# Kernel optimization log

Measured on AMD Instinct MI355X. Metric: run time of the kernel, lower is better.

Reference implementation:

```python
import jax, jax.numpy as jnp
import numpy as np

DIM = 192
NUM_HEADS = 8
EPS = 1e-12  # F.normalize default eps


def setup_inputs() -> dict:
    key = jax.random.key(0)
    ks = jax.random.split(key, 6)
    b, c, h, w = 8, DIM, 128, 128
    scale = 1.0 / np.sqrt(DIM)  # conv2d default init scale (approx)
    return {
        "input": jax.random.normal(ks[0], (b, c, h, w), dtype=jnp.float32),
        "color": jax.random.normal(ks[1], (b, c, h, w), dtype=jnp.float32),
        "Wq": jax.random.normal(ks[2], (DIM, DIM), dtype=jnp.float32) * scale,
        "Wk": jax.random.normal(ks[3], (DIM, DIM), dtype=jnp.float32) * scale,
        "Wv": jax.random.normal(ks[4], (DIM, DIM), dtype=jnp.float32) * scale,
        "Wo": jax.random.normal(ks[5], (DIM, DIM), dtype=jnp.float32) * scale,
    }


def _proj(x, W):
    # 1x1 conv (bias=False) == channel GEMM: [b,c,h,w] x [out,c] -> [b,out,h,w]
    return jnp.einsum('bchw,oc->bohw', x, W)


def _l2norm(x):
    n = jnp.sqrt(jnp.sum(x * x, axis=-1, keepdims=True))
    return x / jnp.maximum(n, EPS)


def reference(input, color, Wq, Wk, Wv, Wo):
    b, c, h, w = input.shape
    head = NUM_HEADS
    dh = c // head
    hw = h * w
    # q from color, k/v from input
    q = _proj(color, Wq).reshape(b, head, dh, hw)
    k = _proj(input, Wk).reshape(b, head, dh, hw)
    v = _proj(input, Wv).reshape(b, head, dh, hw)
    q = _l2norm(q)
    k = _l2norm(k)
    # transposed (channel) attention: [b,head,dh,dh]
    attn = jnp.einsum('bhcn,bhdn->bhcd', q, k)
    attn = jax.nn.softmax(attn, axis=-1)
    out = jnp.einsum('bhcd,bhdn->bhcn', attn, v)  # [b,head,dh,hw]
    out = out.reshape(b, c, h, w)
    return _proj(out, Wo)
```

## Files before the change

kernel.cpp:

```cpp
#include <hip/hip_runtime.h>
#include <hip/hip_bf16.h>


typedef __attribute__((ext_vector_type(4))) float f32x4;
typedef __attribute__((ext_vector_type(8))) short short8;

#define MFMA16(a, b, c) __builtin_amdgcn_mfma_f32_16x16x32_bf16((a), (b), (c), 0, 0, 0)

__device__ __forceinline__ unsigned int pack_rne(float a, float b) {
  unsigned int ua = __float_as_uint(a), ub = __float_as_uint(b);
  ua += 0x7fffu + ((ua >> 16) & 1u);
  ub += 0x7fffu + ((ub >> 16) & 1u);
  return (ua >> 16) | (ub & 0xffff0000u);
}
__device__ __forceinline__ unsigned short bf16u_rne(float x) {
  unsigned int u = __float_as_uint(x);
  u += 0x7fffu + ((u >> 16) & 1u);
  return (unsigned short)(u >> 16);
}
union S8U { short8 s; unsigned int u[4]; };
__device__ __forceinline__ short8 load_cvt8(const float* p) {
  f32x4 x = *(const f32x4*)p;
  f32x4 y = *(const f32x4*)(p + 4);
  S8U r;
  r.u[0] = pack_rne(x[0], x[1]);
  r.u[1] = pack_rne(x[2], x[3]);
  r.u[2] = pack_rne(y[0], y[1]);
  r.u[3] = pack_rne(y[2], y[3]);
  return r.s;
}

#define HW 16384
#define CDIM 192
#define NB 8
#define GSZ (CDIM * CDIM)
#define NTILE 300
#define FSLOT 24576
#define FSKEW 64
#define BROW 80

__global__ void k0_wvt(const float* __restrict__ Wv, unsigned short* __restrict__ WvT) {
  int idx = blockIdx.x * 256 + threadIdx.x;
  if (idx < CDIM * CDIM) {
    int j = idx / CDIM, cp = idx % CDIM;
    WvT[idx] = bf16u_rne(Wv[(size_t)cp * CDIM + j]);
  }
}

__device__ __forceinline__ short8 bfrag(const char* buf, int row, int lg) {
  return *(const short8*)(buf + row * BROW + lg * 16);
}

__device__ __forceinline__ void stageC(const float* __restrict__ ib,
                                       const float* __restrict__ cb, int col0,
                                       char* fdst, int wave, int lane) {
#pragma unroll
  for (int i = 0; i < 2; ++i) {
    const int g = wave * 2 + i;
    const int tensor = g >= 12;
    const int row = (g - (tensor ? 12 : 0)) * 16 + (lane >> 2);
    const float* T = tensor ? cb : ib;
    const float* gp = T + (size_t)row * HW + col0 + (lane & 3) * 4;
    __builtin_amdgcn_global_load_lds(
        (const __attribute__((address_space(1))) void*)gp,
        (__attribute__((address_space(3))) void*)(fdst + g * 1024), 16, 0, 0);
  }
}

template <int W>
__device__ __forceinline__ void pair_step(const char* bb, f32x4 (&acc)[25],
                                          int l15, int lg) {
  const short8 aT = bfrag(bb, W * 16 + l15, lg);
  const short8 aB = bfrag(bb, (23 - W) * 16 + l15, lg);
#pragma unroll
  for (int ct = W; ct < 24; ++ct) {
    const short8 b = bfrag(bb, ct * 16 + l15, lg);
    acc[ct - W] = MFMA16(aT, b, acc[ct - W]);
    if (ct >= 23 - W) acc[ct + 1] = MFMA16(aB, b, acc[ct + 1]);
  }
}

__device__ __forceinline__ void pair_dispatch(int wp, const char* bb,
                                              f32x4 (&acc)[25], int l15, int lg) {
  switch (wp) {
    case 0: pair_step<0>(bb, acc, l15, lg); break;
    case 1: pair_step<1>(bb, acc, l15, lg); break;
    case 2: pair_step<2>(bb, acc, l15, lg); break;
    case 3: pair_step<3>(bb, acc, l15, lg); break;
    case 4: pair_step<4>(bb, acc, l15, lg); break;
    case 5: pair_step<5>(bb, acc, l15, lg); break;
    case 6: pair_step<6>(bb, acc, l15, lg); break;
    case 7: pair_step<7>(bb, acc, l15, lg); break;
    case 8: pair_step<8>(bb, acc, l15, lg); break;
    case 9: pair_step<9>(bb, acc, l15, lg); break;
    case 10: pair_step<10>(bb, acc, l15, lg); break;
    default: pair_step<11>(bb, acc, l15, lg); break;
  }
}

__global__ __launch_bounds__(768) void gram2_k(const float* __restrict__ input,
                                               const float* __restrict__ color,
                                               unsigned long long* __restrict__ part,
                                               int npart, int ncp) {
  __shared__ __align__(16) char fbuf[2][FSLOT + FSKEW];
  __shared__ __align__(16) char bbuf[384 * BROW];
  const int tid = threadIdx.x, wave = tid >> 6, lane = tid & 63;
  const int l15 = lane & 15, lg = (lane >> 4) & 3;
  const int strip = blockIdx.x, b = blockIdx.y;
  const float* ib = input + (size_t)b * CDIM * HW;
  const float* cb = color + (size_t)b * CDIM * HW;
  const int ch0 = strip * ncp * 2;

  f32x4 acc[25];
#pragma unroll
  for (int i = 0; i < 25; ++i) acc[i] = (f32x4){0.f, 0.f, 0.f, 0.f};

  stageC(ib, cb, (ch0 + 0) * 16, fbuf[0], wave, lane);
  stageC(ib, cb, (ch0 + 1) * 16, fbuf[1], wave, lane);

#pragma unroll 1
  for (int cp = 0; cp < ncp; ++cp) {
    __syncthreads();
    {
      const char* sA = fbuf[0];
      const char* sB = fbuf[1];
#pragma unroll
      for (int u0 = 0; u0 < 2; ++u0) {
        const int u = tid + u0 * 768;
        const int zr = u >> 2, sub = u & 3;
        const char* src = (sub < 2 ? sA : sB) + zr * 64 + (sub & 1) * 32;
        f32x4 x = *(const f32x4*)src;
        f32x4 y = *(const f32x4*)(src + 16);
        S8U pk;
        pk.u[0] = pack_rne(x[0], x[1]);
        pk.u[1] = pack_rne(x[2], x[3]);
        pk.u[2] = pack_rne(y[0], y[1]);
        pk.u[3] = pack_rne(y[2], y[3]);
        *(short8*)(bbuf + zr * BROW + sub * 16) = pk.s;
      }
    }
    __syncthreads();
    if (cp + 1 < ncp) {
      stageC(ib, cb, (ch0 + 2 * cp + 2) * 16, fbuf[0], wave, lane);
      stageC(ib, cb, (ch0 + 2 * cp + 3) * 16, fbuf[1], wave, lane);
    }
    pair_dispatch(wave, bbuf, acc, l15, lg);
  }

  unsigned long long* pbase = part + (size_t)(b * npart + strip) * NTILE * 64;
#pragma unroll
  for (int s = 0; s < 25; ++s) {
    const unsigned long long pk =
        (unsigned long long)pack_rne(acc[s][0], acc[s][1]) |
        ((unsigned long long)pack_rne(acc[s][2], acc[s][3]) << 32);
    pbase[(size_t)(wave * 25 + s) * 64 + lane] = pk;
  }
}

template <int NP>
__global__ __launch_bounds__(256) void reduce_k(const unsigned long long* __restrict__ part,
                                                float* __restrict__ G) {
  const int b = blockIdx.y;
  const int T = blockIdx.x * 4 + (threadIdx.x >> 6);
  const int lane = threadIdx.x & 63;
  const unsigned long long* p = part + ((size_t)b * NP * NTILE + T) * 64 + lane;
  unsigned long long v[NP];
#pragma unroll
  for (int s = 0; s < NP; ++s) v[s] = p[(size_t)s * NTILE * 64];
  float s0 = 0.f, s1 = 0.f, s2 = 0.f, s3 = 0.f;
#pragma unroll
  for (int s = 0; s < NP; ++s) {
    const unsigned int lo = (unsigned int)v[s], hi = (unsigned int)(v[s] >> 32);
    s0 += __uint_as_float(lo << 16);
    s1 += __uint_as_float(lo & 0xffff0000u);
    s2 += __uint_as_float(hi << 16);
    s3 += __uint_as_float(hi & 0xffff0000u);
  }
  const int w = T / 25, s = T % 25;
  int rt, ct;
  if (s <= 23 - w) { rt = w; ct = w + s; }
  else { rt = 23 - w; ct = s - 1; }
  int type, gm, gn;
  if (ct < 12) { type = 2; gm = rt; gn = ct; }
  else if (rt < 12) { type = 0; gm = rt; gn = ct - 12; }
  else { type = 1; gm = rt - 12; gn = ct - 12; }
  float* Gm = G + ((size_t)type * NB + b) * GSZ;
  const int l15 = lane & 15, lg = lane >> 4;
  const int row0 = gm * 16 + lg * 4, col = gn * 16 + l15;
  const float sums[4] = {s0, s1, s2, s3};
#pragma unroll
  for (int r = 0; r < 4; ++r) Gm[(size_t)(row0 + r) * CDIM + col] = sums[r];
  if (type != 0 && rt != ct) {
#pragma unroll
    for (int r = 0; r < 4; ++r) Gm[(size_t)col * CDIM + (row0 + r)] = sums[r];
  }
}

__global__ __launch_bounds__(256) void k2a(const float* __restrict__ G,
                                           const float* __restrict__ Wq,
                                           const float* __restrict__ Wk,
                                           float* __restrict__ A_pre,
                                           float* __restrict__ nqk) {
  const int b = blockIdx.x, type = blockIdx.y;
  __shared__ __align__(16) unsigned short Hs[192][200];
  const int tid = threadIdx.x, wave = tid >> 6, lane = tid & 63;
  const int l15 = lane & 15, lg = lane >> 4, row0 = wave * 48;
  const float* W1 = (type == 2) ? Wk : Wq;
  const float* Gm = G + ((size_t)type * NB + b) * GSZ;

  f32x4 acc[3][12];
#pragma unroll
  for (int t = 0; t < 3; t++)
#pragma unroll
    for (int j = 0; j < 12; j++) acc[t][j] = (f32x4){0.f, 0.f, 0.f, 0.f};

  for (int ks = 0; ks < 192; ks += 32) {
    short8 afr[3];
#pragma unroll
    for (int t = 0; t < 3; t++)
      afr[t] = load_cvt8(W1 + (size_t)(row0 + t * 16 + l15) * CDIM + ks + lg * 8);
#pragma unroll
    for (int tj = 0; tj < 12; tj++) {
      short8 bfr = load_cvt8(Gm + (size_t)(tj * 16 + l15) * CDIM + ks + lg * 8);
#pragma unroll
      for (int t = 0; t < 3; t++) acc[t][tj] = MFMA16(afr[t], bfr, acc[t][tj]);
    }
  }
#pragma unroll
  for (int t = 0; t < 3; t++)
#pragma unroll
    for (int tj = 0; tj < 12; tj++)
#pragma unroll
      for (int r = 0; r < 4; r++)
        Hs[row0 + t * 16 + lg * 4 + r][tj * 16 + l15] = bf16u_rne(acc[t][tj][r]);
  __syncthreads();

  if (type == 0) {
    f32x4 a2[3][12];
#pragma unroll
    for (int t = 0; t < 3; t++)
#pragma unroll
      for (int j = 0; j < 12; j++) a2[t][j] = (f32x4){0.f, 0.f, 0.f, 0.f};
    for (int ks = 0; ks < 192; ks += 32) {
      short8 afr[3];
#pragma unroll
      for (int t = 0; t < 3; t++)
        afr[t] = *(const short8*)&Hs[row0 + t * 16 + l15][ks + lg * 8];
#pragma unroll
      for (int tj = 0; tj < 12; tj++) {
        short8 bfr = load_cvt8(Wk + (size_t)(tj * 16 + l15) * CDIM + ks + lg * 8);
#pragma unroll
        for (int t = 0; t < 3; t++) a2[t][tj] = MFMA16(afr[t], bfr, a2[t][tj]);
      }
    }
    float* Ab = A_pre + (size_t)b * GSZ;
#pragma unroll
    for (int t = 0; t < 3; t++)
#pragma unroll
      for (int tj = 0; tj < 12; tj++)
#pragma unroll
        for (int r = 0; r < 4; r++)
          Ab[(size_t)(row0 + t * 16 + lg * 4 + r) * CDIM + tj * 16 + l15] = a2[t][tj][r];
  } else {
    f32x4 a2[3];
#pragma unroll
    for (int t = 0; t < 3; t++) a2[t] = (f32x4){0.f, 0.f, 0.f, 0.f};
    for (int ks = 0; ks < 192; ks += 32) {
#pragma unroll
      for (int t = 0; t < 3; t++) {
        short8 afr = *(const short8*)&Hs[row0 + t * 16 + l15][ks + lg * 8];
        short8 bfr = load_cvt8(W1 + (size_t)(row0 + t * 16 + l15) * CDIM + ks + lg * 8);
        a2[t] = MFMA16(afr, bfr, a2[t]);
      }
    }
    float* dst = nqk + ((size_t)(type - 1) * NB + b) * CDIM;
#pragma unroll
    for (int t = 0; t < 3; t++)
#pragma unroll
      for (int r = 0; r < 4; r++)
        if (lg * 4 + r == l15) dst[row0 + t * 16 + l15] = a2[t][r];
  }
}

__global__ void k2b(const float* __restrict__ A_pre, const float* __restrict__ nqk,
                    float* __restrict__ attnw) {
  const int b = blockIdx.x, tid = threadIdx.x;
  const int h = tid >> 5, r = tid & 31;
  if (r >= 24) return;
  const float* Ab = A_pre + (size_t)b * GSZ;
  const float* nq = nqk + (size_t)b * CDIM;
  const float* nk = nqk + (size_t)(NB + b) * CDIM;
  const int c = h * 24 + r;
  const float qn = rsqrtf(fmaxf(nq[c], 1e-24f));
  float e[24];
  float mx = -1e30f;
#pragma unroll
  for (int d = 0; d < 24; d++) {
    float kn = rsqrtf(fmaxf(nk[h * 24 + d], 1e-24f));
    float l = Ab[(size_t)c * CDIM + h * 24 + d] * qn * kn;
    e[d] = l;
    mx = fmaxf(mx, l);
  }
  float s = 0.f;
#pragma unroll
  for (int d = 0; d < 24; d++) {
    float x = __expf(e[d] - mx);
    e[d] = x;
    s += x;
  }
  const float inv = 1.0f / s;
  float* dst = attnw + (((size_t)b * NB + h) * 24 + r) * 24;
#pragma unroll
  for (int d = 0; d < 24; d++) dst[d] = e[d] * inv;
}

__global__ __launch_bounds__(256) void k3(const float* __restrict__ attnw,
                                          const float* __restrict__ Wo,
                                          const unsigned short* __restrict__ WvT,
                                          unsigned short* __restrict__ Pbf) {
  const int b = blockIdx.x;
  __shared__ __align__(16) unsigned short AT[192][200];
  __shared__ __align__(16) unsigned short Ms[192][200];
  const int tid = threadIdx.x, wave = tid >> 6, lane = tid & 63;
  const int l15 = lane & 15, lg = lane >> 4, row0 = wave * 48;

  unsigned int* ATu = (unsigned int*)&AT[0][0];
  for (int i = tid; i < 192 * 100; i += 256) ATu[i] = 0u;
  __syncthreads();
  const float* at = attnw + (size_t)b * NB * 24 * 24;
  for (int i = tid; i < 4608; i += 256) {
    int h = i / 576, rem = i % 576, c = rem / 24, d = rem % 24;
    AT[h * 24 + d][h * 24 + c] = bf16u_rne(at[(h * 24 + c) * 24 + d]);
  }
  __syncthreads();

  f32x4 acc[3][12];
#pragma unroll
  for (int t = 0; t < 3; t++)
#pragma unroll
    for (int j = 0; j < 12; j++) acc[t][j] = (f32x4){0.f, 0.f, 0.f, 0.f};
  for (int ks = 0; ks < 192; ks += 32) {
    short8 afr[3];
#pragma unroll
    for (int t = 0; t < 3; t++)
      afr[t] = load_cvt8(Wo + (size_t)(row0 + t * 16 + l15) * CDIM + ks + lg * 8);
#pragma unroll
    for (int tj = 0; tj < 12; tj++) {
      short8 bfr = *(const short8*)&AT[tj * 16 + l15][ks + lg * 8];
#pragma unroll
      for (int t = 0; t < 3; t++) acc[t][tj] = MFMA16(afr[t], bfr, acc[t][tj]);
    }
  }
#pragma unroll
  for (int t = 0; t < 3; t++)
#pragma unroll
    for (int tj = 0; tj < 12; tj++)
#pragma unroll
      for (int r = 0; r < 4; r++)
        Ms[row0 + t * 16 + lg * 4 + r][tj * 16 + l15] = bf16u_rne(acc[t][tj][r]);
  __syncthreads();

  f32x4 a2[3][12];
#pragma unroll
  for (int t = 0; t < 3; t++)
#pragma unroll
    for (int j = 0; j < 12; j++) a2[t][j] = (f32x4){0.f, 0.f, 0.f, 0.f};
  for (int ks = 0; ks < 192; ks += 32) {
    short8 afr[3];
#pragma unroll
    for (int t = 0; t < 3; t++)
      afr[t] = *(const short8*)&Ms[row0 + t * 16 + l15][ks + lg * 8];
#pragma unroll
    for (int tj = 0; tj < 12; tj++) {
      short8 bfr = *(const short8*)(WvT + (size_t)(tj * 16 + l15) * CDIM + ks + lg * 8);
#pragma unroll
      for (int t = 0; t < 3; t++) a2[t][tj] = MFMA16(afr[t], bfr, a2[t][tj]);
    }
  }
  unsigned short* Pb = Pbf + (size_t)b * GSZ;
#pragma unroll
  for (int t = 0; t < 3; t++)
#pragma unroll
    for (int tj = 0; tj < 12; tj++)
#pragma unroll
      for (int r = 0; r < 4; r++)
        Pb[(size_t)(row0 + t * 16 + lg * 4 + r) * CDIM + tj * 16 + l15] = bf16u_rne(a2[t][tj][r]);
}

__global__ __launch_bounds__(256) void kD(const unsigned short* __restrict__ Pbf,
                                          const float* __restrict__ input,
                                          float* __restrict__ out) {
  const int nchunk = blockIdx.x, b = blockIdx.y;
  const int n0 = nchunk * 128;
  __shared__ __align__(16) char BsT[128 * 384];
  const int tid = threadIdx.x, wave = tid >> 6, lane = tid & 63;
  const int l15 = lane & 15, lg = lane >> 4, row0 = wave * 48;

  {
    const int n4 = (tid & 31) * 4;
    const int kb0 = (tid >> 5) * 4;
    const float* src = input + (size_t)b * CDIM * HW + n0 + n4;
    f32x4 w[24];
#pragma unroll
    for (int rnd = 0; rnd < 6; ++rnd)
#pragma unroll
      for (int j = 0; j < 4; ++j)
        w[rnd * 4 + j] = *(const f32x4*)(src + (size_t)(kb0 + rnd * 32 + j) * HW);
    __builtin_amdgcn_sched_barrier(0);
    char* bsb = BsT;
#pragma unroll
    for (int rnd = 0; rnd < 6; ++rnd) {
      const int kb = kb0 + rnd * 32;
#pragma unroll
      for (int i = 0; i < 4; ++i) {
        const int n = n4 + i;
        unsigned long long pk =
            (unsigned long long)pack_rne(w[rnd * 4 + 0][i], w[rnd * 4 + 1][i]) |
            ((unsigned long long)pack_rne(w[rnd * 4 + 2][i], w[rnd * 4 + 3][i]) << 32);
        *(unsigned long long*)(bsb + n * 384 + ((kb * 2) ^ ((n & 7) << 4))) = pk;
      }
    }
  }
  __syncthreads();

  f32x4 acc[3][8];
#pragma unroll
  for (int t = 0; t < 3; t++)
#pragma unroll
    for (int j = 0; j < 8; j++) acc[t][j] = (f32x4){0.f, 0.f, 0.f, 0.f};

  const unsigned short* Pb = Pbf + (size_t)b * GSZ;
#pragma unroll 2
  for (int ks = 0; ks < 6; ks++) {
    short8 afr[3];
#pragma unroll
    for (int t = 0; t < 3; t++)
      afr[t] = *(const short8*)(Pb + (size_t)(row0 + t * 16 + l15) * CDIM + ks * 32 + lg * 8);
#pragma unroll
    for (int tn = 0; tn < 8; tn++) {
      const int n = tn * 16 + l15;
      short8 bfr = *(const short8*)(BsT + n * 384 + ((ks * 64 + lg * 16) ^ ((n & 7) << 4)));
#pragma unroll
      for (int t = 0; t < 3; t++) acc[t][tn] = MFMA16(afr[t], bfr, acc[t][tn]);
    }
  }
  float* ob = out + (size_t)b * CDIM * HW + n0;
#pragma unroll
  for (int t = 0; t < 3; t++)
#pragma unroll
    for (int tn = 0; tn < 8; tn++)
#pragma unroll
      for (int r = 0; r < 4; r++) {
        const int m = row0 + t * 16 + lg * 4 + r;
        ob[(size_t)m * HW + tn * 16 + l15] = acc[t][tn][r];
      }
}

extern "C" void kernel_launch(void* const* d_in, const int* in_sizes, int n_in,
                              void* d_out, int out_size, void* d_ws, size_t ws_size,
                              hipStream_t stream) {
  const float* input = (const float*)d_in[0];
  const float* color = (const float*)d_in[1];
  const float* Wq = (const float*)d_in[2];
  const float* Wk = (const float*)d_in[3];
  const float* Wv = (const float*)d_in[4];
  const float* Wo = (const float*)d_in[5];
  float* out = (float*)d_out;
  char* ws = (char*)d_ws;

  const size_t OFF_G = 0;
  const size_t OFF_APRE = 3538944;
  const size_t OFF_NQK = OFF_APRE + 1179648;
  const size_t OFF_ATT = OFF_NQK + 12288;
  const size_t OFF_WVT = OFF_ATT + 147456;
  const size_t OFF_PBF = OFF_WVT + 73728;
  const size_t OFF_PART = OFF_PBF + 589824;

  float* G = (float*)(ws + OFF_G);
  float* A_pre = (float*)(ws + OFF_APRE);
  float* nqk = (float*)(ws + OFF_NQK);
  float* attnw = (float*)(ws + OFF_ATT);
  unsigned short* WvT = (unsigned short*)(ws + OFF_WVT);
  unsigned short* Pbf = (unsigned short*)(ws + OFF_PBF);
  unsigned long long* part = (unsigned long long*)(ws + OFF_PART);

  int npart = 32;
  while (npart > 2 && OFF_PART + (size_t)npart * NB * NTILE * 512 > ws_size) npart >>= 1;
  const int ncp = 512 / npart;

  k0_wvt<<<dim3(144), dim3(256), 0, stream>>>(Wv, WvT);
  gram2_k<<<dim3(npart, NB), dim3(768), 0, stream>>>(input, color, part, npart, ncp);
  switch (npart) {
    case 32: reduce_k<32><<<dim3(75, NB), dim3(256), 0, stream>>>(part, G); break;
    case 16: reduce_k<16><<<dim3(75, NB), dim3(256), 0, stream>>>(part, G); break;
    case 8:  reduce_k<8><<<dim3(75, NB), dim3(256), 0, stream>>>(part, G); break;
    case 4:  reduce_k<4><<<dim3(75, NB), dim3(256), 0, stream>>>(part, G); break;
    default: reduce_k<2><<<dim3(75, NB), dim3(256), 0, stream>>>(part, G); break;
  }
  k2a<<<dim3(NB, 3), dim3(256), 0, stream>>>(G, Wq, Wk, A_pre, nqk);
  k2b<<<dim3(NB), dim3(256), 0, stream>>>(A_pre, nqk, attnw);
  k3<<<dim3(NB), dim3(256), 0, stream>>>(attnw, Wo, WvT, Pbf);
  kD<<<dim3(HW / 128, NB), dim3(256), 0, stream>>>(Pbf, input, out);
}
```

Before: 190.1 us.

## Switch Gram kernel to 32x32x16 MFMA tiles with paired-wave triangular split

After: 190.3 us. Within noise of the previous version (+0.1%).

```diff
diff --git a/kernel.cpp b/kernel.cpp
--- a/kernel.cpp
+++ b/kernel.cpp
@@ -3,9 +3,11 @@
 
 
 typedef __attribute__((ext_vector_type(4))) float f32x4;
+typedef __attribute__((ext_vector_type(16))) float f32x16;
 typedef __attribute__((ext_vector_type(8))) short short8;
 
 #define MFMA16(a, b, c) __builtin_amdgcn_mfma_f32_16x16x32_bf16((a), (b), (c), 0, 0, 0)
+#define MFMA32(a, b, c) __builtin_amdgcn_mfma_f32_32x32x16_bf16((a), (b), (c), 0, 0, 0)
 
 __device__ __forceinline__ unsigned int pack_rne(float a, float b) {
   unsigned int ua = __float_as_uint(a), ub = __float_as_uint(b);
@@ -34,7 +36,7 @@
 #define CDIM 192
 #define NB 8
 #define GSZ (CDIM * CDIM)
-#define NTILE 300
+#define NREC 78
 #define FSLOT 24576
 #define FSKEW 64
 #define BROW 80
@@ -45,10 +47,6 @@
     int j = idx / CDIM, cp = idx % CDIM;
     WvT[idx] = bf16u_rne(Wv[(size_t)cp * CDIM + j]);
   }
-}
-
-__device__ __forceinline__ short8 bfrag(const char* buf, int row, int lg) {
-  return *(const short8*)(buf + row * BROW + lg * 16);
 }
 
 __device__ __forceinline__ void stageC(const float* __restrict__ ib,
@@ -67,34 +65,46 @@
   }
 }
 
-template <int W>
-__device__ __forceinline__ void pair_step(const char* bb, f32x4 (&acc)[25],
-                                          int l15, int lg) {
-  const short8 aT = bfrag(bb, W * 16 + l15, lg);
-  const short8 aB = bfrag(bb, (23 - W) * 16 + l15, lg);
-#pragma unroll
-  for (int ct = W; ct < 24; ++ct) {
-    const short8 b = bfrag(bb, ct * 16 + l15, lg);
-    acc[ct - W] = MFMA16(aT, b, acc[ct - W]);
-    if (ct >= 23 - W) acc[ct + 1] = MFMA16(aB, b, acc[ct + 1]);
-  }
-}
-
-__device__ __forceinline__ void pair_dispatch(int wp, const char* bb,
-                                              f32x4 (&acc)[25], int l15, int lg) {
-  switch (wp) {
-    case 0: pair_step<0>(bb, acc, l15, lg); break;
-    case 1: pair_step<1>(bb, acc, l15, lg); break;
-    case 2: pair_step<2>(bb, acc, l15, lg); break;
-    case 3: pair_step<3>(bb, acc, l15, lg); break;
-    case 4: pair_step<4>(bb, acc, l15, lg); break;
-    case 5: pair_step<5>(bb, acc, l15, lg); break;
-    case 6: pair_step<6>(bb, acc, l15, lg); break;
-    case 7: pair_step<7>(bb, acc, l15, lg); break;
-    case 8: pair_step<8>(bb, acc, l15, lg); break;
-    case 9: pair_step<9>(bb, acc, l15, lg); break;
-    case 10: pair_step<10>(bb, acc, l15, lg); break;
-    default: pair_step<11>(bb, acc, l15, lg); break;
+template <int P, int H>
+__device__ __forceinline__ void pair_step32(const char* bb, f32x16* acc,
+                                            int l31, int hi16, int kb) {
+  constexpr int N0 = 12 - P;
+  constexpr int I0 = H ? 7 : 0;
+  constexpr int I1 = H ? 13 : 7;
+  const short8 aP = *(const short8*)(bb + (P * 32 + l31) * BROW + hi16 + kb);
+  short8 aQ = aP;
+  if constexpr (I1 > N0)
+    aQ = *(const short8*)(bb + ((11 - P) * 32 + l31) * BROW + hi16 + kb);
+#pragma unroll
+  for (int i = I0; i < I1; ++i) {
+    const int ct = (i < N0) ? (P + i) : (i - N0 + 11 - P);
+    const short8 bfr = *(const short8*)(bb + (ct * 32 + l31) * BROW + hi16 + kb);
+    acc[i - I0] = MFMA32((i < N0) ? aP : aQ, bfr, acc[i - I0]);
+  }
+}
+
+template <int P, int H>
+__device__ __forceinline__ void pair_both(const char* bb, f32x16* acc,
+                                          int l31, int hi16) {
+  pair_step32<P, H>(bb, acc, l31, hi16, 0);
+  pair_step32<P, H>(bb, acc, l31, hi16, 32);
+}
+
+__device__ __forceinline__ void pair_dispatch(int wave, const char* bb,
+                                              f32x16* acc, int l31, int hi16) {
+  switch (wave) {
+    case 0: pair_both<0, 0>(bb, acc, l31, hi16); break;
+    case 1: pair_both<0, 1>(bb, acc, l31, hi16); break;
+    case 2: pair_both<1, 0>(bb, acc, l31, hi16); break;
+    case 3: pair_both<1, 1>(bb, acc, l31, hi16); break;
+    case 4: pair_both<2, 0>(bb, acc, l31, hi16); break;
+    case 5: pair_both<2, 1>(bb, acc, l31, hi16); break;
+    case 6: pair_both<3, 0>(bb, acc, l31, hi16); break;
+    case 7: pair_both<3, 1>(bb, acc, l31, hi16); break;
+    case 8: pair_both<4, 0>(bb, acc, l31, hi16); break;
+    case 9: pair_both<4, 1>(bb, acc, l31, hi16); break;
+    case 10: pair_both<5, 0>(bb, acc, l31, hi16); break;
+    default: pair_both<5, 1>(bb, acc, l31, hi16); break;
   }
 }
 
@@ -105,15 +115,17 @@
   __shared__ __align__(16) char fbuf[2][FSLOT + FSKEW];
   __shared__ __align__(16) char bbuf[384 * BROW];
   const int tid = threadIdx.x, wave = tid >> 6, lane = tid & 63;
-  const int l15 = lane & 15, lg = (lane >> 4) & 3;
+  const int l31 = lane & 31, hi16 = (lane >> 5) * 16;
   const int strip = blockIdx.x, b = blockIdx.y;
   const float* ib = input + (size_t)b * CDIM * HW;
   const float* cb = color + (size_t)b * CDIM * HW;
   const int ch0 = strip * ncp * 2;
 
-  f32x4 acc[25];
-#pragma unroll
-  for (int i = 0; i < 25; ++i) acc[i] = (f32x4){0.f, 0.f, 0.f, 0.f};
+  f32x16 acc[7];
+#pragma unroll
+  for (int s = 0; s < 7; ++s)
+#pragma unroll
+    for (int c = 0; c < 16; ++c) acc[s][c] = 0.f;
 
   stageC(ib, cb, (ch0 + 0) * 16, fbuf[0], wave, lane);
   stageC(ib, cb, (ch0 + 1) * 16, fbuf[1], wave, lane);
@@ -144,55 +156,61 @@
       stageC(ib, cb, (ch0 + 2 * cp + 2) * 16, fbuf[0], wave, lane);
       stageC(ib, cb, (ch0 + 2 * cp + 3) * 16, fbuf[1], wave, lane);
     }
-    pair_dispatch(wave, bbuf, acc, l15, lg);
-  }
-
-  unsigned long long* pbase = part + (size_t)(b * npart + strip) * NTILE * 64;
-#pragma unroll
-  for (int s = 0; s < 25; ++s) {
-    const unsigned long long pk =
-        (unsigned long long)pack_rne(acc[s][0], acc[s][1]) |
-        ((unsigned long long)pack_rne(acc[s][2], acc[s][3]) << 32);
-    pbase[(size_t)(wave * 25 + s) * 64 + lane] = pk;
+    pair_dispatch(wave, bbuf, acc, l31, hi16);
+  }
+
+  unsigned long long* pbase = part + (size_t)(b * npart + strip) * NREC * 256;
+  const int p = wave >> 1, H = wave & 1;
+  const int Rbase = p * 13 + (H ? 7 : 0);
+  const int NT = H ? 6 : 7;
+#pragma unroll
+  for (int s = 0; s < 7; ++s) {
+    if (s < NT) {
+#pragma unroll
+      for (int j = 0; j < 4; ++j) {
+        const unsigned long long pk =
+            (unsigned long long)pack_rne(acc[s][4 * j], acc[s][4 * j + 1]) |
+            ((unsigned long long)pack_rne(acc[s][4 * j + 2], acc[s][4 * j + 3]) << 32);
+        pbase[((size_t)(Rbase + s) * 4 + j) * 64 + lane] = pk;
+      }
+    }
   }
 }
 
 template <int NP>
 __global__ __launch_bounds__(256) void reduce_k(const unsigned long long* __restrict__ part,
                                                 float* __restrict__ G) {
-  const int b = blockIdx.y;
-  const int T = blockIdx.x * 4 + (threadIdx.x >> 6);
-  const int lane = threadIdx.x & 63;
-  const unsigned long long* p = part + ((size_t)b * NP * NTILE + T) * 64 + lane;
-  unsigned long long v[NP];
-#pragma unroll
-  for (int s = 0; s < NP; ++s) v[s] = p[(size_t)s * NTILE * 64];
+  const int b = blockIdx.y, T = blockIdx.x;
+  const int j = threadIdx.x >> 6, lane = threadIdx.x & 63;
+  const unsigned long long* p0 =
+      part + ((size_t)b * NP * NREC + T) * 256 + j * 64 + lane;
   float s0 = 0.f, s1 = 0.f, s2 = 0.f, s3 = 0.f;
 #pragma unroll
   for (int s = 0; s < NP; ++s) {
-    const unsigned int lo = (unsigned int)v[s], hi = (unsigned int)(v[s] >> 32);
+    const unsigned long long v = p0[(size_t)s * NREC * 256];
+    const unsigned int lo = (unsigned int)v, hi = (unsigned int)(v >> 32);
     s0 += __uint_as_float(lo << 16);
     s1 += __uint_as_float(lo & 0xffff0000u);
     s2 += __uint_as_float(hi << 16);
     s3 += __uint_as_float(hi & 0xffff0000u);
   }
-  const int w = T / 25, s = T % 25;
-  int rt, ct;
-  if (s <= 23 - w) { rt = w; ct = w + s; }
-  else { rt = 23 - w; ct = s - 1; }
-  int type, gm, gn;
-  if (ct < 12) { type = 2; gm = rt; gn = ct; }
-  else if (rt < 12) { type = 0; gm = rt; gn = ct - 12; }
-  else { type = 1; gm = rt - 12; gn = ct - 12; }
-  float* Gm = G + ((size_t)type * NB + b) * GSZ;
-  const int l15 = lane & 15, lg = lane >> 4;
-  const int row0 = gm * 16 + lg * 4, col = gn * 16 + l15;
+  const int p = T / 13, i = T % 13;
+  const int N0 = 12 - p;
+  const int rt = (i < N0) ? p : 11 - p;
+  const int ct = (i < N0) ? p + i : i - N0 + 11 - p;
+  const int hi5 = lane >> 5, col = lane & 31;
+  const int zc = ct * 32 + col;
   const float sums[4] = {s0, s1, s2, s3};
 #pragma unroll
-  for (int r = 0; r < 4; ++r) Gm[(size_t)(row0 + r) * CDIM + col] = sums[r];
-  if (type != 0 && rt != ct) {
-#pragma unroll
-    for (int r = 0; r < 4; ++r) Gm[(size_t)col * CDIM + (row0 + r)] = sums[r];
+  for (int m = 0; m < 4; ++m) {
+    const int zr = rt * 32 + m + 8 * j + 4 * hi5;
+    int type, gr, gc;
+    if (zc < 192) { type = 2; gr = zr; gc = zc; }
+    else if (zr < 192) { type = 0; gr = zr; gc = zc - 192; }
+    else { type = 1; gr = zr - 192; gc = zc - 192; }
+    float* Gm = G + ((size_t)type * NB + b) * GSZ;
+    Gm[(size_t)gr * CDIM + gc] = sums[m];
+    if (type != 0 && rt != ct) Gm[(size_t)gc * CDIM + gr] = sums[m];
   }
 }
 
@@ -485,17 +503,17 @@
   unsigned long long* part = (unsigned long long*)(ws + OFF_PART);
 
   int npart = 32;
-  while (npart > 2 && OFF_PART + (size_t)npart * NB * NTILE * 512 > ws_size) npart >>= 1;
+  while (npart > 2 && OFF_PART + (size_t)npart * NB * NREC * 2048 > ws_size) npart >>= 1;
   const int ncp = 512 / npart;
 
   k0_wvt<<<dim3(144), dim3(256), 0, stream>>>(Wv, WvT);
   gram2_k<<<dim3(npart, NB), dim3(768), 0, stream>>>(input, color, part, npart, ncp);
   switch (npart) {
-    case 32: reduce_k<32><<<dim3(75, NB), dim3(256), 0, stream>>>(part, G); break;
-    case 16: reduce_k<16><<<dim3(75, NB), dim3(256), 0, stream>>>(part, G); break;
-    case 8:  reduce_k<8><<<dim3(75, NB), dim3(256), 0, stream>>>(part, G); break;
-    case 4:  reduce_k<4><<<dim3(75, NB), dim3(256), 0, stream>>>(part, G); break;
-    default: reduce_k<2><<<dim3(75, NB), dim3(256), 0, stream>>>(part, G); break;
+    case 32: reduce_k<32><<<dim3(NREC, NB), dim3(256), 0, stream>>>(part, G); break;
+    case 16: reduce_k<16><<<dim3(NREC, NB), dim3(256), 0, stream>>>(part, G); break;
+    case 8:  reduce_k<8><<<dim3(NREC, NB), dim3(256), 0, stream>>>(part, G); break;
+    case 4:  reduce_k<4><<<dim3(NREC, NB), dim3(256), 0, stream>>>(part, G); break;
+    default: reduce_k<2><<<dim3(NREC, NB), dim3(256), 0, stream>>>(part, G); break;
   }
   k2a<<<dim3(NB, 3), dim3(256), 0, stream>>>(G, Wq, Wk, A_pre, nqk);
   k2b<<<dim3(NB), dim3(256), 0, stream>>>(A_pre, nqk, attnw);
```

## Load Gram tiles via register prefetch, widen K step, reuse output as partials

Applied to the files above, without the earlier changes.

New measurement: 186.0 us. 1.02x faster.

```diff
diff --git a/kernel.cpp b/kernel.cpp
--- a/kernel.cpp
+++ b/kernel.cpp
@@ -35,9 +35,9 @@
 #define NB 8
 #define GSZ (CDIM * CDIM)
 #define NTILE 300
-#define FSLOT 24576
-#define FSKEW 64
-#define BROW 80
+#define NPART 32
+#define NPH 8
+#define BROW 144
 
 __global__ void k0_wvt(const float* __restrict__ Wv, unsigned short* __restrict__ WvT) {
   int idx = blockIdx.x * 256 + threadIdx.x;
@@ -47,36 +47,23 @@
   }
 }
 
-__device__ __forceinline__ short8 bfrag(const char* buf, int row, int lg) {
-  return *(const short8*)(buf + row * BROW + lg * 16);
-}
-
-__device__ __forceinline__ void stageC(const float* __restrict__ ib,
-                                       const float* __restrict__ cb, int col0,
-                                       char* fdst, int wave, int lane) {
-#pragma unroll
-  for (int i = 0; i < 2; ++i) {
-    const int g = wave * 2 + i;
-    const int tensor = g >= 12;
-    const int row = (g - (tensor ? 12 : 0)) * 16 + (lane >> 2);
-    const float* T = tensor ? cb : ib;
-    const float* gp = T + (size_t)row * HW + col0 + (lane & 3) * 4;
-    __builtin_amdgcn_global_load_lds(
-        (const __attribute__((address_space(1))) void*)gp,
-        (__attribute__((address_space(3))) void*)(fdst + g * 1024), 16, 0, 0);
-  }
+__device__ __forceinline__ short8 bfrag(const char* buf, int row, int lg, int ks2) {
+  return *(const short8*)(buf + row * BROW + ks2 * 64 + lg * 16);
 }
 
 template <int W>
 __device__ __forceinline__ void pair_step(const char* bb, f32x4 (&acc)[25],
                                           int l15, int lg) {
-  const short8 aT = bfrag(bb, W * 16 + l15, lg);
-  const short8 aB = bfrag(bb, (23 - W) * 16 + l15, lg);
-#pragma unroll
-  for (int ct = W; ct < 24; ++ct) {
-    const short8 b = bfrag(bb, ct * 16 + l15, lg);
-    acc[ct - W] = MFMA16(aT, b, acc[ct - W]);
-    if (ct >= 23 - W) acc[ct + 1] = MFMA16(aB, b, acc[ct + 1]);
+#pragma unroll
+  for (int ks2 = 0; ks2 < 2; ++ks2) {
+    const short8 aT = bfrag(bb, W * 16 + l15, lg, ks2);
+    const short8 aB = bfrag(bb, (23 - W) * 16 + l15, lg, ks2);
+#pragma unroll
+    for (int ct = W; ct < 24; ++ct) {
+      const short8 b = bfrag(bb, ct * 16 + l15, lg, ks2);
+      acc[ct - W] = MFMA16(aT, b, acc[ct - W]);
+      if (ct >= 23 - W) acc[ct + 1] = MFMA16(aB, b, acc[ct + 1]);
+    }
   }
 }
 
@@ -100,54 +87,77 @@
 
 __global__ __launch_bounds__(768) void gram2_k(const float* __restrict__ input,
                                                const float* __restrict__ color,
-                                               unsigned long long* __restrict__ part,
-                                               int npart, int ncp) {
-  __shared__ __align__(16) char fbuf[2][FSLOT + FSKEW];
+                                               unsigned long long* __restrict__ part) {
   __shared__ __align__(16) char bbuf[384 * BROW];
   const int tid = threadIdx.x, wave = tid >> 6, lane = tid & 63;
   const int l15 = lane & 15, lg = (lane >> 4) & 3;
   const int strip = blockIdx.x, b = blockIdx.y;
-  const float* ib = input + (size_t)b * CDIM * HW;
-  const float* cb = color + (size_t)b * CDIM * HW;
-  const int ch0 = strip * ncp * 2;
+  const int zrow = tid >> 1, half = tid & 1;
+  const float* src = ((zrow < 192) ? (input + (size_t)zrow * HW)
+                                   : (color + (size_t)(zrow - 192) * HW)) +
+                     (size_t)b * CDIM * HW;
+  const int col00 = strip * NPH * 64 + half * 32;
 
   f32x4 acc[25];
 #pragma unroll
   for (int i = 0; i < 25; ++i) acc[i] = (f32x4){0.f, 0.f, 0.f, 0.f};
 
-  stageC(ib, cb, (ch0 + 0) * 16, fbuf[0], wave, lane);
-  stageC(ib, cb, (ch0 + 1) * 16, fbuf[1], wave, lane);
+  f32x4 v0, v1, v2, v3, v4, v5, v6, v7;
+  {
+    const float* p = src + col00;
+    v0 = *(const f32x4*)(p);
+    v1 = *(const f32x4*)(p + 4);
+    v2 = *(const f32x4*)(p + 8);
+    v3 = *(const f32x4*)(p + 12);
+    v4 = *(const f32x4*)(p + 16);
+    v5 = *(const f32x4*)(p + 20);
+    v6 = *(const f32x4*)(p + 24);
+    v7 = *(const f32x4*)(p + 28);
+  }
 
 #pragma unroll 1
-  for (int cp = 0; cp < ncp; ++cp) {
+  for (int ph = 0; ph < NPH; ++ph) {
     __syncthreads();
     {
-      const char* sA = fbuf[0];
-      const char* sB = fbuf[1];
-#pragma unroll
-      for (int u0 = 0; u0 < 2; ++u0) {
-        const int u = tid + u0 * 768;
-        const int zr = u >> 2, sub = u & 3;
-        const char* src = (sub < 2 ? sA : sB) + zr * 64 + (sub & 1) * 32;
-        f32x4 x = *(const f32x4*)src;
-        f32x4 y = *(const f32x4*)(src + 16);
-        S8U pk;
-        pk.u[0] = pack_rne(x[0], x[1]);
-        pk.u[1] = pack_rne(x[2], x[3]);
-        pk.u[2] = pack_rne(y[0], y[1]);
-        pk.u[3] = pack_rne(y[2], y[3]);
-        *(short8*)(bbuf + zr * BROW + sub * 16) = pk.s;
-      }
+      char* dst = bbuf + zrow * BROW + half * 64;
+      S8U pk;
+      pk.u[0] = pack_rne(v0[0], v0[1]);
+      pk.u[1] = pack_rne(v0[2], v0[3]);
+      pk.u[2] = pack_rne(v1[0], v1[1]);
+      pk.u[3] = pack_rne(v1[2], v1[3]);
+      *(short8*)(dst) = pk.s;
+      pk.u[0] = pack_rne(v2[0], v2[1]);
+      pk.u[1] = pack_rne(v2[2], v2[3]);
+      pk.u[2] = pack_rne(v3[0], v3[1]);
+      pk.u[3] = pack_rne(v3[2], v3[3]);
+      *(short8*)(dst + 16) = pk.s;
+      pk.u[0] = pack_rne(v4[0], v4[1]);
+      pk.u[1] = pack_rne(v4[2], v4[3]);
+      pk.u[2] = pack_rne(v5[0], v5[1]);
+      pk.u[3] = pack_rne(v5[2], v5[3]);
+      *(short8*)(dst + 32) = pk.s;
+      pk.u[0] = pack_rne(v6[0], v6[1]);
+      pk.u[1] = pack_rne(v6[2], v6[3]);
+      pk.u[2] = pack_rne(v7[0], v7[1]);
+      pk.u[3] = pack_rne(v7[2], v7[3]);
+      *(short8*)(dst + 48) = pk.s;
     }
     __syncthreads();
-    if (cp + 1 < ncp) {
-      stageC(ib, cb, (ch0 + 2 * cp + 2) * 16, fbuf[0], wave, lane);
-      stageC(ib, cb, (ch0 + 2 * cp + 3) * 16, fbuf[1], wave, lane);
+    if (ph + 1 < NPH) {
+      const float* p = src + col00 + (ph + 1) * 64;
+      v0 = *(const f32x4*)(p);
+      v1 = *(const f32x4*)(p + 4);
+      v2 = *(const f32x4*)(p + 8);
+      v3 = *(const f32x4*)(p + 12);
+      v4 = *(const f32x4*)(p + 16);
+      v5 = *(const f32x4*)(p + 20);
+      v6 = *(const f32x4*)(p + 24);
+      v7 = *(const f32x4*)(p + 28);
     }
     pair_dispatch(wave, bbuf, acc, l15, lg);
   }
 
-  unsigned long long* pbase = part + (size_t)(b * npart + strip) * NTILE * 64;
+  unsigned long long* pbase = part + (size_t)(b * NPART + strip) * NTILE * 64;
 #pragma unroll
   for (int s = 0; s < 25; ++s) {
     const unsigned long long pk =
@@ -474,7 +484,6 @@
   const size_t OFF_ATT = OFF_NQK + 12288;
   const size_t OFF_WVT = OFF_ATT + 147456;
   const size_t OFF_PBF = OFF_WVT + 73728;
-  const size_t OFF_PART = OFF_PBF + 589824;
 
   float* G = (float*)(ws + OFF_G);
   float* A_pre = (float*)(ws + OFF_APRE);
@@ -482,21 +491,12 @@
   float* attnw = (float*)(ws + OFF_ATT);
   unsigned short* WvT = (unsigned short*)(ws + OFF_WVT);
   unsigned short* Pbf = (unsigned short*)(ws + OFF_PBF);
-  unsigned long long* part = (unsigned long long*)(ws + OFF_PART);
-
-  int npart = 32;
-  while (npart > 2 && OFF_PART + (size_t)npart * NB * NTILE * 512 > ws_size) npart >>= 1;
-  const int ncp = 512 / npart;
+
+  unsigned long long* part = (unsigned long long*)d_out;
 
   k0_wvt<<<dim3(144), dim3(256), 0, stream>>>(Wv, WvT);
-  gram2_k<<<dim3(npart, NB), dim3(768), 0, stream>>>(input, color, part, npart, ncp);
-  switch (npart) {
-    case 32: reduce_k<32><<<dim3(75, NB), dim3(256), 0, stream>>>(part, G); break;
-    case 16: reduce_k<16><<<dim3(75, NB), dim3(256), 0, stream>>>(part, G); break;
-    case 8:  reduce_k<8><<<dim3(75, NB), dim3(256), 0, stream>>>(part, G); break;
-    case 4:  reduce_k<4><<<dim3(75, NB), dim3(256), 0, stream>>>(part, G); break;
-    default: reduce_k<2><<<dim3(75, NB), dim3(256), 0, stream>>>(part, G); break;
-  }
+  gram2_k<<<dim3(NPART, NB), dim3(768), 0, stream>>>(input, color, part);
+  reduce_k<NPART><<<dim3(75, NB), dim3(256), 0, stream>>>(part, G);
   k2a<<<dim3(NB, 3), dim3(256), 0, stream>>>(G, Wq, Wk, A_pre, nqk);
   k2b<<<dim3(NB), dim3(256), 0, stream>>>(A_pre, nqk, attnw);
   k3<<<dim3(NB), dim3(256), 0, stream>>>(attnw, Wo, WvT, Pbf);
```
